# Optimization experiments

Measured on AMD Instinct MI355X. Metric: run time of the kernel, lower is better.

Reference implementation:

```python
import jax, jax.numpy as jnp
import numpy as np

B = 262144      # batch
DIN = 100       # input covariate dim (cfg_density[0][0])
H = 64          # hidden dim
G = 10          # num_grid -> density output dim G+1
NH = 5          # number of dosage-bucket heads in Multi_head


def setup_inputs() -> dict:
    key = jax.random.key(0)
    ks = jax.random.split(key, 16)
    s = 0.05
    return {
        "dosage": jax.random.uniform(ks[0], (B,), dtype=jnp.float32),
        "x": jax.random.normal(ks[1], (B, DIN), dtype=jnp.float32),
        # density feature MLP (two Linear+ReLU layers)
        "dW0": jax.random.normal(ks[2], (DIN, H), dtype=jnp.float32) * s,
        "db0": jax.random.normal(ks[3], (H,), dtype=jnp.float32) * s,
        "dW1": jax.random.normal(ks[4], (H, H), dtype=jnp.float32) * s,
        "db1": jax.random.normal(ks[5], (H,), dtype=jnp.float32) * s,
        # Density_Block: Linear(H -> G+1) then softmax + grid interpolation
        "dbW": jax.random.normal(ks[6], (H, G + 1), dtype=jnp.float32) * s,
        "dbB": jax.random.normal(ks[7], (G + 1,), dtype=jnp.float32) * s,
        # Multi_head: 5 structurally identical heads, params stacked on axis 0
        # layer0: Treat_Linear(64 -> 64, relu, istreat=1)
        "W0": jax.random.normal(ks[8], (NH, H, H), dtype=jnp.float32) * s,
        "tw0": jax.random.normal(ks[9], (NH, H), dtype=jnp.float32) * s,
        "b0": jax.random.normal(ks[10], (NH, H), dtype=jnp.float32) * s,
        # layer1 (last): Treat_Linear(64 -> 1, no act, istreat=1)
        "W1": jax.random.normal(ks[11], (NH, H, 1), dtype=jnp.float32) * s,
        "tw1": jax.random.normal(ks[12], (NH, 1), dtype=jnp.float32) * s,
        "b1": jax.random.normal(ks[13], (NH, 1), dtype=jnp.float32) * s,
    }


def reference(dosage, x, dW0, db0, dW1, db1, dbW, dbB, W0, tw0, b0, W1, tw1, b1):
    # hidden feature MLP
    hidden = jax.nn.relu(x @ dW0 + db0)
    hidden = jax.nn.relu(hidden @ dW1 + db1)            # [B, H]

    # ---- Density_Block: softmax over grid, dual gather + linear interpolation
    p = jax.nn.softmax(hidden @ dbW + dbB, axis=1)      # [B, G+1]
    tB = dosage * G
    U = jnp.ceil(tB)
    inter = 1.0 - (U - tB)                              # fractional position in cell
    Ui = U.astype(jnp.int32)
    Li = Ui - 1
    Li = Li + (Li < 0).astype(jnp.int32)                # clamp L=-1 -> 0
    pL = jnp.take_along_axis(p, Li[:, None], axis=1)[:, 0]
    pU = jnp.take_along_axis(p, Ui[:, None], axis=1)[:, 0]
    g = pL + (pU - pL) * inter                          # [B]

    # ---- Multi_head: 5 heads on dosage buckets [0,.2),[.2,.4),...,[.8,1.)
    t = dosage
    # layer0: out = feat @ W + t * tw + b, relu; compute all heads, select later
    h0 = jax.nn.relu(
        jnp.einsum('bi,hio->bho', hidden, W0)
        + t[:, None, None] * tw0[None]
        + b0[None]
    )                                                   # [B, NH, H]
    # last layer: no activation
    out1 = (jnp.einsum('bho,hoj->bhj', h0, W1)
            + t[:, None, None] * tw1[None]
            + b1[None])                                 # [B, NH, 1]
    bucket = jnp.clip(jnp.floor(t * NH).astype(jnp.int32), 0, NH - 1)
    Q = jnp.take_along_axis(out1, bucket[:, None, None], axis=1)[:, 0, :]  # [B, 1]
    return g, Q
```

## Files before the change

### kernel.cpp

```cpp
#include <hip/hip_runtime.h>

typedef __attribute__((ext_vector_type(8))) short  short8;
typedef __attribute__((ext_vector_type(4))) float  floatx4;
typedef __attribute__((ext_vector_type(4))) int    intx4;

constexpr int DIN = 100;
constexpr int H   = 64;
constexpr int G   = 10;
constexpr int NH  = 5;
constexpr int MWG = 128;
constexpr int HP  = 72;
constexpr int PBP = 20;

constexpr int NF_DW0 = 16, NF_DW1 = 8, NF_DBW = 2;
constexpr int NF_LIN = NF_DW0 + NF_DW1 + NF_DBW;
constexpr int NF_TOT = NF_LIN + 40;

__device__ __forceinline__ unsigned short f2bf_rne(float f) {
    union { float f; unsigned u; } v{f};
    unsigned r = v.u + 0x7FFF + ((v.u >> 16) & 1);
    return (unsigned short)(r >> 16);
}

__device__ __forceinline__ short8 pack8(const float* f) {
    intx4 p;
    #pragma unroll
    for (int j = 0; j < 4; ++j) {
        unsigned a = __float_as_uint(f[2 * j])     + 0x8000u;
        unsigned b = __float_as_uint(f[2 * j + 1]) + 0x8000u;
        p[j] = (int)((b & 0xFFFF0000u) | (a >> 16));
    }
    union { intx4 i; short8 s; } u; u.i = p;
    return u.s;
}

__device__ __forceinline__ unsigned pack2bf(float a, float b) {
    unsigned ua = __float_as_uint(a) + 0x8000u;
    unsigned ub = __float_as_uint(b) + 0x8000u;
    return (ua >> 16) | (ub & 0xFFFF0000u);
}

__device__ __forceinline__ short8 ldfrag(const unsigned short* __restrict__ ws,
                                         int f, int lane) {
    return *(const short8*)(ws + (size_t)(f * 64 + lane) * 8);
}

__device__ __forceinline__ void bar_lgkm() {
    asm volatile("s_waitcnt lgkmcnt(0)" ::: "memory");
    __builtin_amdgcn_s_barrier();
    asm volatile("" ::: "memory");
}

__global__ __launch_bounds__(64) void pack_kernel(
    const float* __restrict__ dW0, const float* __restrict__ dW1,
    const float* __restrict__ dbW, const float* __restrict__ W0,
    unsigned short* __restrict__ ws)
{
    const int f = blockIdx.x;
    const int lane = threadIdx.x;
    const int q = lane >> 4, cl = lane & 15;
    float v[8];
    if (f < NF_DW0) {
        int c = f >> 2, g = f & 3;
        #pragma unroll
        for (int j = 0; j < 8; ++j) {
            int k = c * 32 + q * 8 + j, n = g * 16 + cl;
            v[j] = (k < DIN) ? dW0[k * H + n] : 0.0f;
        }
    } else if (f < NF_DW0 + NF_DW1) {
        int r = f - NF_DW0; int c = r >> 2, g = r & 3;
        #pragma unroll
        for (int j = 0; j < 8; ++j) {
            int k = c * 32 + q * 8 + j, n = g * 16 + cl;
            v[j] = dW1[k * H + n];
        }
    } else if (f < NF_LIN) {
        int c = f - (NF_DW0 + NF_DW1);
        #pragma unroll
        for (int j = 0; j < 8; ++j) {
            int k = c * 32 + q * 8 + j, n = cl;
            v[j] = (n <= G) ? dbW[k * (G + 1) + n] : 0.0f;
        }
    } else {
        int r = f - NF_LIN; int h = r >> 3; r &= 7; int c = r >> 2, g = r & 3;
        #pragma unroll
        for (int j = 0; j < 8; ++j) {
            int k = c * 32 + q * 8 + j, n = g * 16 + cl;
            v[j] = W0[(h * H + k) * H + n];
        }
    }
    short8 s;
    #pragma unroll
    for (int j = 0; j < 8; ++j) s[j] = (short)f2bf_rne(v[j]);
    *(short8*)(ws + (size_t)(f * 64 + lane) * 8) = s;
}

__global__ __launch_bounds__(256, 3) void drnet_mfma(
    const float* __restrict__ dosage, const float* __restrict__ x,
    const float* __restrict__ db0, const float* __restrict__ db1,
    const float* __restrict__ dbB,
    const float* __restrict__ tw0, const float* __restrict__ b0,
    const float* __restrict__ W1, const float* __restrict__ tw1,
    const float* __restrict__ b1,
    const unsigned short* __restrict__ wsfrag,
    float* __restrict__ outg, float* __restrict__ outq)
{
    __shared__ unsigned short hbuf[MWG * HP];
    __shared__ float          pbuf[4][16][PBP];
    __shared__ int            perm[MWG];
    __shared__ float          tbuf[MWG];
    __shared__ unsigned char  bkbuf[MWG];
    __shared__ float          qbuf[MWG];
    __shared__ int            hist[NH];
    __shared__ int            offs[NH];

    const int tid  = threadIdx.x;
    const int wave = tid >> 6, lane = tid & 63;
    const int q = lane >> 4, cl = lane & 15;
    const int rowbase = blockIdx.x * MWG + wave * 32;
    unsigned short* hb = hbuf + wave * 32 * HP;

    floatx4 tvs[2];
    #pragma unroll
    for (int mt = 0; mt < 2; ++mt)
        tvs[mt] = *(const floatx4*)(dosage + rowbase + mt * 16 + 4 * q);
    floatx4 xv[2][7];
    #pragma unroll
    for (int mt = 0; mt < 2; ++mt) {
        const float* xr = x + (size_t)(rowbase + mt * 16 + cl) * DIN;
        #pragma unroll
        for (int cch = 0; cch < 3; ++cch) {
            xv[mt][2 * cch]     = *(const floatx4*)(xr + cch * 32 + q * 8);
            xv[mt][2 * cch + 1] = *(const floatx4*)(xr + cch * 32 + q * 8 + 4);
        }
        xv[mt][6] = (q == 0) ? *(const floatx4*)(xr + 96) : (floatx4)0.0f;
    }

    if (tid < NH) hist[tid] = 0;
    bar_lgkm();
    {
        float t8[2][4];
        int   bk8[2][4];
        #pragma unroll
        for (int mt = 0; mt < 2; ++mt)
            #pragma unroll
            for (int r = 0; r < 4; ++r) {
                float t = tvs[mt][r];
                t8[mt][r] = t;
                int bk = (int)floorf(t * (float)NH);
                bk8[mt][r] = min(max(bk, 0), NH - 1);
            }
        if (cl == 0) {
            #pragma unroll
            for (int mt = 0; mt < 2; ++mt)
                #pragma unroll
                for (int r = 0; r < 4; ++r)
                    atomicAdd(&hist[bk8[mt][r]], 1);
        }
        bar_lgkm();
        if (tid == 0) {
            int a = 0;
            #pragma unroll
            for (int h = 0; h < NH; ++h) { offs[h] = a; a += hist[h]; }
        }
        bar_lgkm();
        if (cl == 0) {
            #pragma unroll
            for (int mt = 0; mt < 2; ++mt)
                #pragma unroll
                for (int r = 0; r < 4; ++r) {
                    const int bk  = bk8[mt][r];
                    const int pos = atomicAdd(&offs[bk], 1);
                    perm[pos]  = wave * 32 + mt * 16 + 4 * q + r;
                    tbuf[pos]  = t8[mt][r];
                    bkbuf[pos] = (unsigned char)bk;
                }
        }
    }

    {
        short8 a1[2][4];
        #pragma unroll
        for (int mt = 0; mt < 2; ++mt)
            #pragma unroll
            for (int cch = 0; cch < 4; ++cch) {
                float f[8];
                if (cch < 3) {
                    #pragma unroll
                    for (int j = 0; j < 4; ++j) {
                        f[j]     = xv[mt][2 * cch][j];
                        f[4 + j] = xv[mt][2 * cch + 1][j];
                    }
                } else {
                    #pragma unroll
                    for (int j = 0; j < 4; ++j) {
                        f[j]     = xv[mt][6][j];
                        f[4 + j] = 0.0f;
                    }
                }
                a1[mt][cch] = pack8(f);
            }
        floatx4 acc[2][4];
        #pragma unroll
        for (int mt = 0; mt < 2; ++mt)
            #pragma unroll
            for (int g = 0; g < 4; ++g) acc[mt][g] = (floatx4)0.0f;
        #pragma unroll
        for (int cch = 0; cch < 4; ++cch)
            #pragma unroll
            for (int g = 0; g < 4; ++g) {
                short8 bf = ldfrag(wsfrag, cch * 4 + g, lane);
                acc[0][g] = __builtin_amdgcn_mfma_f32_16x16x32_bf16(bf, a1[0][cch], acc[0][g], 0, 0, 0);
                acc[1][g] = __builtin_amdgcn_mfma_f32_16x16x32_bf16(bf, a1[1][cch], acc[1][g], 0, 0, 0);
            }
        #pragma unroll
        for (int mt = 0; mt < 2; ++mt)
            #pragma unroll
            for (int g = 0; g < 4; ++g) {
                floatx4 bias = *(const floatx4*)(db0 + g * 16 + 4 * q);
                float v0 = fmaxf(acc[mt][g][0] + bias[0], 0.0f);
                float v1 = fmaxf(acc[mt][g][1] + bias[1], 0.0f);
                float v2 = fmaxf(acc[mt][g][2] + bias[2], 0.0f);
                float v3 = fmaxf(acc[mt][g][3] + bias[3], 0.0f);
                *(uint2*)(hb + (size_t)(mt * 16 + cl) * HP + g * 16 + 4 * q) =
                    make_uint2(pack2bf(v0, v1), pack2bf(v2, v3));
            }
    }

    {
        short8 a2[2][2];
        #pragma unroll
        for (int mt = 0; mt < 2; ++mt)
            #pragma unroll
            for (int cch = 0; cch < 2; ++cch)
                a2[mt][cch] = *(const short8*)(hb + (mt * 16 + cl) * HP + cch * 32 + q * 8);
        floatx4 acc[2][4];
        #pragma unroll
        for (int mt = 0; mt < 2; ++mt)
            #pragma unroll
            for (int g = 0; g < 4; ++g) acc[mt][g] = (floatx4)0.0f;
        #pragma unroll
        for (int cch = 0; cch < 2; ++cch)
            #pragma unroll
            for (int g = 0; g < 4; ++g) {
                short8 bf = ldfrag(wsfrag, NF_DW0 + cch * 4 + g, lane);
                acc[0][g] = __builtin_amdgcn_mfma_f32_16x16x32_bf16(bf, a2[0][cch], acc[0][g], 0, 0, 0);
                acc[1][g] = __builtin_amdgcn_mfma_f32_16x16x32_bf16(bf, a2[1][cch], acc[1][g], 0, 0, 0);
            }
        #pragma unroll
        for (int mt = 0; mt < 2; ++mt)
            #pragma unroll
            for (int g = 0; g < 4; ++g) {
                floatx4 bias = *(const floatx4*)(db1 + g * 16 + 4 * q);
                float v0 = fmaxf(acc[mt][g][0] + bias[0], 0.0f);
                float v1 = fmaxf(acc[mt][g][1] + bias[1], 0.0f);
                float v2 = fmaxf(acc[mt][g][2] + bias[2], 0.0f);
                float v3 = fmaxf(acc[mt][g][3] + bias[3], 0.0f);
                *(uint2*)(hb + (size_t)(mt * 16 + cl) * HP + g * 16 + 4 * q) =
                    make_uint2(pack2bf(v0, v1), pack2bf(v2, v3));
            }
    }

    {
        float tden[2];
        #pragma unroll
        for (int mt = 0; mt < 2; ++mt)
            tden[mt] = dosage[rowbase + mt * 16 + cl];
        short8 af[2][2];
        #pragma unroll
        for (int mt = 0; mt < 2; ++mt)
            #pragma unroll
            for (int cch = 0; cch < 2; ++cch)
                af[mt][cch] = *(const short8*)(hb + (mt * 16 + cl) * HP + cch * 32 + q * 8);
        floatx4 accd[2];
        accd[0] = (floatx4)0.0f; accd[1] = (floatx4)0.0f;
        #pragma unroll
        for (int cch = 0; cch < 2; ++cch) {
            short8 bf = ldfrag(wsfrag, NF_DW0 + NF_DW1 + cch, lane);
            #pragma unroll
            for (int mt = 0; mt < 2; ++mt)
                accd[mt] = __builtin_amdgcn_mfma_f32_16x16x32_bf16(bf, af[mt][cch], accd[mt], 0, 0, 0);
        }
        #pragma unroll
        for (int mt = 0; mt < 2; ++mt) {
            floatx4 ev;
            float sp = 0.0f;
            #pragma unroll
            for (int r = 0; r < 4; ++r) {
                const int gd = 4 * q + r;
                float e = (gd <= G) ? __expf(accd[mt][r] + dbB[gd]) : 0.0f;
                ev[r] = e;
                sp += e;
            }
            float s = sp;
            s += __shfl_xor(s, 16); s += __shfl_xor(s, 32);
            *(floatx4*)(&pbuf[wave][cl][4 * q]) = ev;
            const float t  = tden[mt];
            const float tB = t * (float)G;
            const float U  = ceilf(tB);
            const float inter = 1.0f - (U - tB);
            int Ui = (int)U; int Li = Ui - 1; if (Li < 0) Li = 0;
            const float pL = pbuf[wave][cl][Li];
            const float pU = pbuf[wave][cl][Ui];
            if (q == 0)
                outg[rowbase + mt * 16 + cl] = (pL + (pU - pL) * inter) / s;
        }
    }

    __syncthreads();
    {
        short8 ag[2][2];
        int    prow[2], bkme[2], blo[2], bhi[2];
        float  tme[2];
        #pragma unroll
        for (int mt = 0; mt < 2; ++mt) {
            const int base = (wave * 2 + mt) * 16;
            prow[mt] = perm[base + cl];
            ag[mt][0] = *(const short8*)(hbuf + prow[mt] * HP + q * 8);
            ag[mt][1] = *(const short8*)(hbuf + prow[mt] * HP + 32 + q * 8);
            tme[mt]  = tbuf[base + cl];
            bkme[mt] = bkbuf[base + cl];
            blo[mt]  = bkbuf[base];
            bhi[mt]  = bkbuf[base + 15];
        }
        #pragma unroll
        for (int mt = 0; mt < 2; ++mt) {
            float qp = 0.0f;
            #pragma unroll 1
            for (int h = blo[mt]; h <= bhi[mt]; ++h) {
                floatx4 acch[4];
                #pragma unroll
                for (int g = 0; g < 4; ++g) acch[g] = (floatx4)0.0f;
                #pragma unroll
                for (int cch = 0; cch < 2; ++cch)
                    #pragma unroll
                    for (int g = 0; g < 4; ++g) {
                        short8 bf = ldfrag(wsfrag, NF_LIN + h * 8 + cch * 4 + g, lane);
                        acch[g] = __builtin_amdgcn_mfma_f32_16x16x32_bf16(bf, ag[mt][cch], acch[g], 0, 0, 0);
                    }
                if (bkme[mt] == h) {
                    #pragma unroll
                    for (int g = 0; g < 4; ++g) {
                        const int off = h * H + g * 16 + 4 * q;
                        floatx4 tw0v = *(const floatx4*)(tw0 + off);
                        floatx4 b0v  = *(const floatx4*)(b0  + off);
                        floatx4 w1v  = *(const floatx4*)(W1  + off);
                        #pragma unroll
                        for (int r = 0; r < 4; ++r)
                            qp += fmaxf(acch[g][r] + tme[mt] * tw0v[r] + b0v[r], 0.0f) * w1v[r];
                    }
                }
            }
            qp += __shfl_xor(qp, 16); qp += __shfl_xor(qp, 32);
            if (q == 0)
                qbuf[prow[mt]] = qp + tme[mt] * tw1[bkme[mt]] + b1[bkme[mt]];
        }
    }

    __syncthreads();
    if (tid < MWG / 4) {
        floatx4 v = *(const floatx4*)(qbuf + tid * 4);
        *(floatx4*)(outq + blockIdx.x * MWG + tid * 4) = v;
    }
}

extern "C" void kernel_launch(void* const* d_in, const int* in_sizes, int n_in,
                              void* d_out, int out_size, void* d_ws, size_t ws_size,
                              hipStream_t stream) {
    const float* dosage = (const float*)d_in[0];
    const float* x      = (const float*)d_in[1];
    const float* dW0    = (const float*)d_in[2];
    const float* db0    = (const float*)d_in[3];
    const float* dW1    = (const float*)d_in[4];
    const float* db1    = (const float*)d_in[5];
    const float* dbW    = (const float*)d_in[6];
    const float* dbB    = (const float*)d_in[7];
    const float* W0     = (const float*)d_in[8];
    const float* tw0    = (const float*)d_in[9];
    const float* b0     = (const float*)d_in[10];
    const float* W1     = (const float*)d_in[11];
    const float* tw1    = (const float*)d_in[12];
    const float* b1     = (const float*)d_in[13];

    const int Btot = in_sizes[0];
    float* outg = (float*)d_out;
    float* outq = outg + Btot;
    unsigned short* ws = (unsigned short*)d_ws;

    pack_kernel<<<NF_TOT, 64, 0, stream>>>(dW0, dW1, dbW, W0, ws);
    drnet_mfma<<<Btot / MWG, 256, 0, stream>>>(dosage, x, db0, db1, dbB,
                                               tw0, b0, W1, tw1, b1,
                                               ws, outg, outq);
}
```

Measured before the change: 198.7 us.

## Process four row tiles per block with prefetch of next tile's inputs

After: 264.2 us. 33.0% more time.

```diff
diff --git a/kernel.cpp b/kernel.cpp
--- a/kernel.cpp
+++ b/kernel.cpp
@@ -9,6 +9,7 @@
 constexpr int G   = 10;
 constexpr int NH  = 5;
 constexpr int MWG = 128;
+constexpr int TPB = 4;
 constexpr int HP  = 72;
 constexpr int PBP = 20;
 
@@ -117,250 +118,277 @@
     const int tid  = threadIdx.x;
     const int wave = tid >> 6, lane = tid & 63;
     const int q = lane >> 4, cl = lane & 15;
-    const int rowbase = blockIdx.x * MWG + wave * 32;
     unsigned short* hb = hbuf + wave * 32 * HP;
 
+    const int tilebase = blockIdx.x * TPB;
+
     floatx4 tvs[2];
-    #pragma unroll
-    for (int mt = 0; mt < 2; ++mt)
-        tvs[mt] = *(const floatx4*)(dosage + rowbase + mt * 16 + 4 * q);
     floatx4 xv[2][7];
-    #pragma unroll
-    for (int mt = 0; mt < 2; ++mt) {
-        const float* xr = x + (size_t)(rowbase + mt * 16 + cl) * DIN;
-        #pragma unroll
-        for (int cch = 0; cch < 3; ++cch) {
-            xv[mt][2 * cch]     = *(const floatx4*)(xr + cch * 32 + q * 8);
-            xv[mt][2 * cch + 1] = *(const floatx4*)(xr + cch * 32 + q * 8 + 4);
-        }
-        xv[mt][6] = (q == 0) ? *(const floatx4*)(xr + 96) : (floatx4)0.0f;
+    {
+        const int rowbase = tilebase * MWG + wave * 32;
+        #pragma unroll
+        for (int mt = 0; mt < 2; ++mt)
+            tvs[mt] = *(const floatx4*)(dosage + rowbase + mt * 16 + 4 * q);
+        #pragma unroll
+        for (int mt = 0; mt < 2; ++mt) {
+            const float* xr = x + (size_t)(rowbase + mt * 16 + cl) * DIN;
+            #pragma unroll
+            for (int cch = 0; cch < 3; ++cch) {
+                xv[mt][2 * cch]     = *(const floatx4*)(xr + cch * 32 + q * 8);
+                xv[mt][2 * cch + 1] = *(const floatx4*)(xr + cch * 32 + q * 8 + 4);
+            }
+            xv[mt][6] = (q == 0) ? *(const floatx4*)(xr + 96) : (floatx4)0.0f;
+        }
     }
 
-    if (tid < NH) hist[tid] = 0;
-    bar_lgkm();
-    {
-        float t8[2][4];
-        int   bk8[2][4];
-        #pragma unroll
-        for (int mt = 0; mt < 2; ++mt)
-            #pragma unroll
-            for (int r = 0; r < 4; ++r) {
-                float t = tvs[mt][r];
-                t8[mt][r] = t;
-                int bk = (int)floorf(t * (float)NH);
-                bk8[mt][r] = min(max(bk, 0), NH - 1);
-            }
-        if (cl == 0) {
-            #pragma unroll
-            for (int mt = 0; mt < 2; ++mt)
-                #pragma unroll
-                for (int r = 0; r < 4; ++r)
-                    atomicAdd(&hist[bk8[mt][r]], 1);
-        }
+    #pragma unroll 1
+    for (int t = 0; t < TPB; ++t) {
+        const int rowbase = (tilebase + t) * MWG + wave * 32;
+
+        if (tid < NH) hist[tid] = 0;
         bar_lgkm();
-        if (tid == 0) {
-            int a = 0;
-            #pragma unroll
-            for (int h = 0; h < NH; ++h) { offs[h] = a; a += hist[h]; }
-        }
+        {
+            float t8[2][4];
+            int   bk8[2][4];
+            #pragma unroll
+            for (int mt = 0; mt < 2; ++mt)
+                #pragma unroll
+                for (int r = 0; r < 4; ++r) {
+                    float tt = tvs[mt][r];
+                    t8[mt][r] = tt;
+                    int bk = (int)floorf(tt * (float)NH);
+                    bk8[mt][r] = min(max(bk, 0), NH - 1);
+                }
+            if (cl == 0) {
+                #pragma unroll
+                for (int mt = 0; mt < 2; ++mt)
+                    #pragma unroll
+                    for (int r = 0; r < 4; ++r)
+                        atomicAdd(&hist[bk8[mt][r]], 1);
+            }
+            bar_lgkm();
+            if (tid == 0) {
+                int a = 0;
+                #pragma unroll
+                for (int h = 0; h < NH; ++h) { offs[h] = a; a += hist[h]; }
+            }
+            bar_lgkm();
+            if (cl == 0) {
+                #pragma unroll
+                for (int mt = 0; mt < 2; ++mt)
+                    #pragma unroll
+                    for (int r = 0; r < 4; ++r) {
+                        const int bk  = bk8[mt][r];
+                        const int pos = atomicAdd(&offs[bk], 1);
+                        perm[pos]  = wave * 32 + mt * 16 + 4 * q + r;
+                        tbuf[pos]  = t8[mt][r];
+                        bkbuf[pos] = (unsigned char)bk;
+                    }
+            }
+        }
+
+        {
+            short8 a1[2][4];
+            #pragma unroll
+            for (int mt = 0; mt < 2; ++mt)
+                #pragma unroll
+                for (int cch = 0; cch < 4; ++cch) {
+                    float f[8];
+                    if (cch < 3) {
+                        #pragma unroll
+                        for (int j = 0; j < 4; ++j) {
+                            f[j]     = xv[mt][2 * cch][j];
+                            f[4 + j] = xv[mt][2 * cch + 1][j];
+                        }
+                    } else {
+                        #pragma unroll
+                        for (int j = 0; j < 4; ++j) {
+                            f[j]     = xv[mt][6][j];
+                            f[4 + j] = 0.0f;
+                        }
+                    }
+                    a1[mt][cch] = pack8(f);
+                }
+            floatx4 acc[2][4];
+            #pragma unroll
+            for (int mt = 0; mt < 2; ++mt)
+                #pragma unroll
+                for (int g = 0; g < 4; ++g) acc[mt][g] = (floatx4)0.0f;
+            #pragma unroll
+            for (int cch = 0; cch < 4; ++cch)
+                #pragma unroll
+                for (int g = 0; g < 4; ++g) {
+                    short8 bf = ldfrag(wsfrag, cch * 4 + g, lane);
+                    acc[0][g] = __builtin_amdgcn_mfma_f32_16x16x32_bf16(bf, a1[0][cch], acc[0][g], 0, 0, 0);
+                    acc[1][g] = __builtin_amdgcn_mfma_f32_16x16x32_bf16(bf, a1[1][cch], acc[1][g], 0, 0, 0);
+                }
+            #pragma unroll
+            for (int mt = 0; mt < 2; ++mt)
+                #pragma unroll
+                for (int g = 0; g < 4; ++g) {
+                    floatx4 bias = *(const floatx4*)(db0 + g * 16 + 4 * q);
+                    float v0 = fmaxf(acc[mt][g][0] + bias[0], 0.0f);
+                    float v1 = fmaxf(acc[mt][g][1] + bias[1], 0.0f);
+                    float v2 = fmaxf(acc[mt][g][2] + bias[2], 0.0f);
+                    float v3 = fmaxf(acc[mt][g][3] + bias[3], 0.0f);
+                    *(uint2*)(hb + (size_t)(mt * 16 + cl) * HP + g * 16 + 4 * q) =
+                        make_uint2(pack2bf(v0, v1), pack2bf(v2, v3));
+                }
+        }
+
+        {
+            short8 a2[2][2];
+            #pragma unroll
+            for (int mt = 0; mt < 2; ++mt)
+                #pragma unroll
+                for (int cch = 0; cch < 2; ++cch)
+                    a2[mt][cch] = *(const short8*)(hb + (mt * 16 + cl) * HP + cch * 32 + q * 8);
+            floatx4 acc[2][4];
+            #pragma unroll
+            for (int mt = 0; mt < 2; ++mt)
+                #pragma unroll
+                for (int g = 0; g < 4; ++g) acc[mt][g] = (floatx4)0.0f;
+            #pragma unroll
+            for (int cch = 0; cch < 2; ++cch)
+                #pragma unroll
+                for (int g = 0; g < 4; ++g) {
+                    short8 bf = ldfrag(wsfrag, NF_DW0 + cch * 4 + g, lane);
+                    acc[0][g] = __builtin_amdgcn_mfma_f32_16x16x32_bf16(bf, a2[0][cch], acc[0][g], 0, 0, 0);
+                    acc[1][g] = __builtin_amdgcn_mfma_f32_16x16x32_bf16(bf, a2[1][cch], acc[1][g], 0, 0, 0);
+                }
+            #pragma unroll
+            for (int mt = 0; mt < 2; ++mt)
+                #pragma unroll
+                for (int g = 0; g < 4; ++g) {
+                    floatx4 bias = *(const floatx4*)(db1 + g * 16 + 4 * q);
+                    float v0 = fmaxf(acc[mt][g][0] + bias[0], 0.0f);
+                    float v1 = fmaxf(acc[mt][g][1] + bias[1], 0.0f);
+                    float v2 = fmaxf(acc[mt][g][2] + bias[2], 0.0f);
+                    float v3 = fmaxf(acc[mt][g][3] + bias[3], 0.0f);
+                    *(uint2*)(hb + (size_t)(mt * 16 + cl) * HP + g * 16 + 4 * q) =
+                        make_uint2(pack2bf(v0, v1), pack2bf(v2, v3));
+                }
+        }
+
+        {
+            float tden[2];
+            #pragma unroll
+            for (int mt = 0; mt < 2; ++mt)
+                tden[mt] = dosage[rowbase + mt * 16 + cl];
+            short8 af[2][2];
+            #pragma unroll
+            for (int mt = 0; mt < 2; ++mt)
+                #pragma unroll
+                for (int cch = 0; cch < 2; ++cch)
+                    af[mt][cch] = *(const short8*)(hb + (mt * 16 + cl) * HP + cch * 32 + q * 8);
+            floatx4 accd[2];
+            accd[0] = (floatx4)0.0f; accd[1] = (floatx4)0.0f;
+            #pragma unroll
+            for (int cch = 0; cch < 2; ++cch) {
+                short8 bf = ldfrag(wsfrag, NF_DW0 + NF_DW1 + cch, lane);
+                #pragma unroll
+                for (int mt = 0; mt < 2; ++mt)
+                    accd[mt] = __builtin_amdgcn_mfma_f32_16x16x32_bf16(bf, af[mt][cch], accd[mt], 0, 0, 0);
+            }
+            #pragma unroll
+            for (int mt = 0; mt < 2; ++mt) {
+                floatx4 ev;
+                float sp = 0.0f;
+                #pragma unroll
+                for (int r = 0; r < 4; ++r) {
+                    const int gd = 4 * q + r;
+                    float e = (gd <= G) ? __expf(accd[mt][r] + dbB[gd]) : 0.0f;
+                    ev[r] = e;
+                    sp += e;
+                }
+                float s = sp;
+                s += __shfl_xor(s, 16); s += __shfl_xor(s, 32);
+                *(floatx4*)(&pbuf[wave][cl][4 * q]) = ev;
+                const float tt = tden[mt];
+                const float tB = tt * (float)G;
+                const float U  = ceilf(tB);
+                const float inter = 1.0f - (U - tB);
+                int Ui = (int)U; int Li = Ui - 1; if (Li < 0) Li = 0;
+                const float pL = pbuf[wave][cl][Li];
+                const float pU = pbuf[wave][cl][Ui];
+                if (q == 0)
+                    outg[rowbase + mt * 16 + cl] = (pL + (pU - pL) * inter) / s;
+            }
+        }
+
         bar_lgkm();
-        if (cl == 0) {
-            #pragma unroll
-            for (int mt = 0; mt < 2; ++mt)
-                #pragma unroll
-                for (int r = 0; r < 4; ++r) {
-                    const int bk  = bk8[mt][r];
-                    const int pos = atomicAdd(&offs[bk], 1);
-                    perm[pos]  = wave * 32 + mt * 16 + 4 * q + r;
-                    tbuf[pos]  = t8[mt][r];
-                    bkbuf[pos] = (unsigned char)bk;
-                }
-        }
-    }
-
-    {
-        short8 a1[2][4];
-        #pragma unroll
-        for (int mt = 0; mt < 2; ++mt)
-            #pragma unroll
-            for (int cch = 0; cch < 4; ++cch) {
-                float f[8];
-                if (cch < 3) {
+
+        if (t + 1 < TPB) {
+            const int rbn = rowbase + MWG;
+            #pragma unroll
+            for (int mt = 0; mt < 2; ++mt)
+                tvs[mt] = *(const floatx4*)(dosage + rbn + mt * 16 + 4 * q);
+            #pragma unroll
+            for (int mt = 0; mt < 2; ++mt) {
+                const float* xr = x + (size_t)(rbn + mt * 16 + cl) * DIN;
+                #pragma unroll
+                for (int cch = 0; cch < 3; ++cch) {
+                    xv[mt][2 * cch]     = *(const floatx4*)(xr + cch * 32 + q * 8);
+                    xv[mt][2 * cch + 1] = *(const floatx4*)(xr + cch * 32 + q * 8 + 4);
+                }
+                xv[mt][6] = (q == 0) ? *(const floatx4*)(xr + 96) : (floatx4)0.0f;
+            }
+        }
+
+        {
+            short8 ag[2][2];
+            int    prow[2], bkme[2], blo[2], bhi[2];
+            float  tme[2];
+            #pragma unroll
+            for (int mt = 0; mt < 2; ++mt) {
+                const int base = (wave * 2 + mt) * 16;
+                prow[mt] = perm[base + cl];
+                ag[mt][0] = *(const short8*)(hbuf + prow[mt] * HP + q * 8);
+                ag[mt][1] = *(const short8*)(hbuf + prow[mt] * HP + 32 + q * 8);
+                tme[mt]  = tbuf[base + cl];
+                bkme[mt] = bkbuf[base + cl];
+                blo[mt]  = bkbuf[base];
+                bhi[mt]  = bkbuf[base + 15];
+            }
+            #pragma unroll
+            for (int mt = 0; mt < 2; ++mt) {
+                float qp = 0.0f;
+                #pragma unroll 1
+                for (int h = blo[mt]; h <= bhi[mt]; ++h) {
+                    floatx4 acch[4];
                     #pragma unroll
-                    for (int j = 0; j < 4; ++j) {
-                        f[j]     = xv[mt][2 * cch][j];
-                        f[4 + j] = xv[mt][2 * cch + 1][j];
+                    for (int g = 0; g < 4; ++g) acch[g] = (floatx4)0.0f;
+                    #pragma unroll
+                    for (int cch = 0; cch < 2; ++cch)
+                        #pragma unroll
+                        for (int g = 0; g < 4; ++g) {
+                            short8 bf = ldfrag(wsfrag, NF_LIN + h * 8 + cch * 4 + g, lane);
+                            acch[g] = __builtin_amdgcn_mfma_f32_16x16x32_bf16(bf, ag[mt][cch], acch[g], 0, 0, 0);
+                        }
+                    if (bkme[mt] == h) {
+                        #pragma unroll
+                        for (int g = 0; g < 4; ++g) {
+                            const int off = h * H + g * 16 + 4 * q;
+                            floatx4 tw0v = *(const floatx4*)(tw0 + off);
+                            floatx4 b0v  = *(const floatx4*)(b0  + off);
+                            floatx4 w1v  = *(const floatx4*)(W1  + off);
+                            #pragma unroll
+                            for (int r = 0; r < 4; ++r)
+                                qp += fmaxf(acch[g][r] + tme[mt] * tw0v[r] + b0v[r], 0.0f) * w1v[r];
+                        }
                     }
-                } else {
-                    #pragma unroll
-                    for (int j = 0; j < 4; ++j) {
-                        f[j]     = xv[mt][6][j];
-                        f[4 + j] = 0.0f;
-                    }
-                }
-                a1[mt][cch] = pack8(f);
-            }
-        floatx4 acc[2][4];
-        #pragma unroll
-        for (int mt = 0; mt < 2; ++mt)
-            #pragma unroll
-            for (int g = 0; g < 4; ++g) acc[mt][g] = (floatx4)0.0f;
-        #pragma unroll
-        for (int cch = 0; cch < 4; ++cch)
-            #pragma unroll
-            for (int g = 0; g < 4; ++g) {
-                short8 bf = ldfrag(wsfrag, cch * 4 + g, lane);
-                acc[0][g] = __builtin_amdgcn_mfma_f32_16x16x32_bf16(bf, a1[0][cch], acc[0][g], 0, 0, 0);
-                acc[1][g] = __builtin_amdgcn_mfma_f32_16x16x32_bf16(bf, a1[1][cch], acc[1][g], 0, 0, 0);
-            }
-        #pragma unroll
-        for (int mt = 0; mt < 2; ++mt)
-            #pragma unroll
-            for (int g = 0; g < 4; ++g) {
-                floatx4 bias = *(const floatx4*)(db0 + g * 16 + 4 * q);
-                float v0 = fmaxf(acc[mt][g][0] + bias[0], 0.0f);
-                float v1 = fmaxf(acc[mt][g][1] + bias[1], 0.0f);
-                float v2 = fmaxf(acc[mt][g][2] + bias[2], 0.0f);
-                float v3 = fmaxf(acc[mt][g][3] + bias[3], 0.0f);
-                *(uint2*)(hb + (size_t)(mt * 16 + cl) * HP + g * 16 + 4 * q) =
-                    make_uint2(pack2bf(v0, v1), pack2bf(v2, v3));
-            }
-    }
-
-    {
-        short8 a2[2][2];
-        #pragma unroll
-        for (int mt = 0; mt < 2; ++mt)
-            #pragma unroll
-            for (int cch = 0; cch < 2; ++cch)
-                a2[mt][cch] = *(const short8*)(hb + (mt * 16 + cl) * HP + cch * 32 + q * 8);
-        floatx4 acc[2][4];
-        #pragma unroll
-        for (int mt = 0; mt < 2; ++mt)
-            #pragma unroll
-            for (int g = 0; g < 4; ++g) acc[mt][g] = (floatx4)0.0f;
-        #pragma unroll
-        for (int cch = 0; cch < 2; ++cch)
-            #pragma unroll
-            for (int g = 0; g < 4; ++g) {
-                short8 bf = ldfrag(wsfrag, NF_DW0 + cch * 4 + g, lane);
-                acc[0][g] = __builtin_amdgcn_mfma_f32_16x16x32_bf16(bf, a2[0][cch], acc[0][g], 0, 0, 0);
-                acc[1][g] = __builtin_amdgcn_mfma_f32_16x16x32_bf16(bf, a2[1][cch], acc[1][g], 0, 0, 0);
-            }
-        #pragma unroll
-        for (int mt = 0; mt < 2; ++mt)
-            #pragma unroll
-            for (int g = 0; g < 4; ++g) {
-                floatx4 bias = *(const floatx4*)(db1 + g * 16 + 4 * q);
-                float v0 = fmaxf(acc[mt][g][0] + bias[0], 0.0f);
-                float v1 = fmaxf(acc[mt][g][1] + bias[1], 0.0f);
-                float v2 = fmaxf(acc[mt][g][2] + bias[2], 0.0f);
-                float v3 = fmaxf(acc[mt][g][3] + bias[3], 0.0f);
-                *(uint2*)(hb + (size_t)(mt * 16 + cl) * HP + g * 16 + 4 * q) =
-                    make_uint2(pack2bf(v0, v1), pack2bf(v2, v3));
-            }
-    }
-
-    {
-        float tden[2];
-        #pragma unroll
-        for (int mt = 0; mt < 2; ++mt)
-            tden[mt] = dosage[rowbase + mt * 16 + cl];
-        short8 af[2][2];
-        #pragma unroll
-        for (int mt = 0; mt < 2; ++mt)
-            #pragma unroll
-            for (int cch = 0; cch < 2; ++cch)
-                af[mt][cch] = *(const short8*)(hb + (mt * 16 + cl) * HP + cch * 32 + q * 8);
-        floatx4 accd[2];
-        accd[0] = (floatx4)0.0f; accd[1] = (floatx4)0.0f;
-        #pragma unroll
-        for (int cch = 0; cch < 2; ++cch) {
-            short8 bf = ldfrag(wsfrag, NF_DW0 + NF_DW1 + cch, lane);
-            #pragma unroll
-            for (int mt = 0; mt < 2; ++mt)
-                accd[mt] = __builtin_amdgcn_mfma_f32_16x16x32_bf16(bf, af[mt][cch], accd[mt], 0, 0, 0);
-        }
-        #pragma unroll
-        for (int mt = 0; mt < 2; ++mt) {
-            floatx4 ev;
-            float sp = 0.0f;
-            #pragma unroll
-            for (int r = 0; r < 4; ++r) {
-                const int gd = 4 * q + r;
-                float e = (gd <= G) ? __expf(accd[mt][r] + dbB[gd]) : 0.0f;
-                ev[r] = e;
-                sp += e;
-            }
-            float s = sp;
-            s += __shfl_xor(s, 16); s += __shfl_xor(s, 32);
-            *(floatx4*)(&pbuf[wave][cl][4 * q]) = ev;
-            const float t  = tden[mt];
-            const float tB = t * (float)G;
-            const float U  = ceilf(tB);
-            const float inter = 1.0f - (U - tB);
-            int Ui = (int)U; int Li = Ui - 1; if (Li < 0) Li = 0;
-            const float pL = pbuf[wave][cl][Li];
-            const float pU = pbuf[wave][cl][Ui];
-            if (q == 0)
-                outg[rowbase + mt * 16 + cl] = (pL + (pU - pL) * inter) / s;
-        }
-    }
-
-    __syncthreads();
-    {
-        short8 ag[2][2];
-        int    prow[2], bkme[2], blo[2], bhi[2];
-        float  tme[2];
-        #pragma unroll
-        for (int mt = 0; mt < 2; ++mt) {
-            const int base = (wave * 2 + mt) * 16;
-            prow[mt] = perm[base + cl];
-            ag[mt][0] = *(const short8*)(hbuf + prow[mt] * HP + q * 8);
-            ag[mt][1] = *(const short8*)(hbuf + prow[mt] * HP + 32 + q * 8);
-            tme[mt]  = tbuf[base + cl];
-            bkme[mt] = bkbuf[base + cl];
-            blo[mt]  = bkbuf[base];
-            bhi[mt]  = bkbuf[base + 15];
-        }
-        #pragma unroll
-        for (int mt = 0; mt < 2; ++mt) {
-            float qp = 0.0f;
-            #pragma unroll 1
-            for (int h = blo[mt]; h <= bhi[mt]; ++h) {
-                floatx4 acch[4];
-                #pragma unroll
-                for (int g = 0; g < 4; ++g) acch[g] = (floatx4)0.0f;
-                #pragma unroll
-                for (int cch = 0; cch < 2; ++cch)
-                    #pragma unroll
-                    for (int g = 0; g < 4; ++g) {
-                        short8 bf = ldfrag(wsfrag, NF_LIN + h * 8 + cch * 4 + g, lane);
-                        acch[g] = __builtin_amdgcn_mfma_f32_16x16x32_bf16(bf, ag[mt][cch], acch[g], 0, 0, 0);
-                    }
-                if (bkme[mt] == h) {
-                    #pragma unroll
-                    for (int g = 0; g < 4; ++g) {
-                        const int off = h * H + g * 16 + 4 * q;
-                        floatx4 tw0v = *(const floatx4*)(tw0 + off);
-                        floatx4 b0v  = *(const floatx4*)(b0  + off);
-                        floatx4 w1v  = *(const floatx4*)(W1  + off);
-                        #pragma unroll
-                        for (int r = 0; r < 4; ++r)
-                            qp += fmaxf(acch[g][r] + tme[mt] * tw0v[r] + b0v[r], 0.0f) * w1v[r];
-                    }
-                }
-            }
-            qp += __shfl_xor(qp, 16); qp += __shfl_xor(qp, 32);
-            if (q == 0)
-                qbuf[prow[mt]] = qp + tme[mt] * tw1[bkme[mt]] + b1[bkme[mt]];
-        }
-    }
-
-    __syncthreads();
-    if (tid < MWG / 4) {
-        floatx4 v = *(const floatx4*)(qbuf + tid * 4);
-        *(floatx4*)(outq + blockIdx.x * MWG + tid * 4) = v;
+                }
+                qp += __shfl_xor(qp, 16); qp += __shfl_xor(qp, 32);
+                if (q == 0)
+                    qbuf[prow[mt]] = qp + tme[mt] * tw1[bkme[mt]] + b1[bkme[mt]];
+            }
+        }
+
+        bar_lgkm();
+        if (tid < MWG / 4) {
+            floatx4 v = *(const floatx4*)(qbuf + tid * 4);
+            *(floatx4*)(outq + (tilebase + t) * MWG + tid * 4) = v;
+        }
     }
 }
 
@@ -388,7 +416,7 @@
     unsigned short* ws = (unsigned short*)d_ws;
 
     pack_kernel<<<NF_TOT, 64, 0, stream>>>(dW0, dW1, dbW, W0, ws);
-    drnet_mfma<<<Btot / MWG, 256, 0, stream>>>(dosage, x, db0, db1, dbB,
-                                               tw0, b0, W1, tw1, b1,
-                                               ws, outg, outq);
-}
+    drnet_mfma<<<Btot / (MWG * TPB), 256, 0, stream>>>(dosage, x, db0, db1, dbB,
+                                                       tw0, b0, W1, tw1, b1,
+                                                       ws, outg, outq);
+}
```

## Replace block-wide atomic bucket sort with per-wave ballot sort, drop barriers

Applied to the files above, without the earlier changes.

Result: slower. 228.0 us (+14.8%).

```diff
diff --git a/kernel.cpp b/kernel.cpp
--- a/kernel.cpp
+++ b/kernel.cpp
@@ -43,12 +43,6 @@
 __device__ __forceinline__ short8 ldfrag(const unsigned short* __restrict__ ws,
                                          int f, int lane) {
     return *(const short8*)(ws + (size_t)(f * 64 + lane) * 8);
-}
-
-__device__ __forceinline__ void bar_lgkm() {
-    asm volatile("s_waitcnt lgkmcnt(0)" ::: "memory");
-    __builtin_amdgcn_s_barrier();
-    asm volatile("" ::: "memory");
 }
 
 __global__ __launch_bounds__(64) void pack_kernel(
@@ -95,7 +89,7 @@
     *(short8*)(ws + (size_t)(f * 64 + lane) * 8) = s;
 }
 
-__global__ __launch_bounds__(256, 3) void drnet_mfma(
+__global__ __launch_bounds__(256, 6) void drnet_mfma(
     const float* __restrict__ dosage, const float* __restrict__ x,
     const float* __restrict__ db0, const float* __restrict__ db1,
     const float* __restrict__ dbB,
@@ -105,25 +99,19 @@
     const unsigned short* __restrict__ wsfrag,
     float* __restrict__ outg, float* __restrict__ outq)
 {
-    __shared__ unsigned short hbuf[MWG * HP];
+    __shared__ unsigned short hbuf[4][32 * HP];
     __shared__ float          pbuf[4][16][PBP];
-    __shared__ int            perm[MWG];
-    __shared__ float          tbuf[MWG];
-    __shared__ unsigned char  bkbuf[MWG];
-    __shared__ float          qbuf[MWG];
-    __shared__ int            hist[NH];
-    __shared__ int            offs[NH];
+    __shared__ int            perm[4][32];
+    __shared__ float          tbufs[4][32];
+    __shared__ int            bks[4][32];
+    __shared__ float          qbufs[4][32];
 
     const int tid  = threadIdx.x;
     const int wave = tid >> 6, lane = tid & 63;
     const int q = lane >> 4, cl = lane & 15;
     const int rowbase = blockIdx.x * MWG + wave * 32;
-    unsigned short* hb = hbuf + wave * 32 * HP;
-
-    floatx4 tvs[2];
-    #pragma unroll
-    for (int mt = 0; mt < 2; ++mt)
-        tvs[mt] = *(const floatx4*)(dosage + rowbase + mt * 16 + 4 * q);
+    unsigned short* hb = hbuf[wave];
+
     floatx4 xv[2][7];
     #pragma unroll
     for (int mt = 0; mt < 2; ++mt) {
@@ -136,45 +124,28 @@
         xv[mt][6] = (q == 0) ? *(const floatx4*)(xr + 96) : (floatx4)0.0f;
     }
 
-    if (tid < NH) hist[tid] = 0;
-    bar_lgkm();
-    {
-        float t8[2][4];
-        int   bk8[2][4];
-        #pragma unroll
-        for (int mt = 0; mt < 2; ++mt)
-            #pragma unroll
-            for (int r = 0; r < 4; ++r) {
-                float t = tvs[mt][r];
-                t8[mt][r] = t;
-                int bk = (int)floorf(t * (float)NH);
-                bk8[mt][r] = min(max(bk, 0), NH - 1);
-            }
-        if (cl == 0) {
-            #pragma unroll
-            for (int mt = 0; mt < 2; ++mt)
-                #pragma unroll
-                for (int r = 0; r < 4; ++r)
-                    atomicAdd(&hist[bk8[mt][r]], 1);
-        }
-        bar_lgkm();
-        if (tid == 0) {
-            int a = 0;
-            #pragma unroll
-            for (int h = 0; h < NH; ++h) { offs[h] = a; a += hist[h]; }
-        }
-        bar_lgkm();
-        if (cl == 0) {
-            #pragma unroll
-            for (int mt = 0; mt < 2; ++mt)
-                #pragma unroll
-                for (int r = 0; r < 4; ++r) {
-                    const int bk  = bk8[mt][r];
-                    const int pos = atomicAdd(&offs[bk], 1);
-                    perm[pos]  = wave * 32 + mt * 16 + 4 * q + r;
-                    tbuf[pos]  = t8[mt][r];
-                    bkbuf[pos] = (unsigned char)bk;
-                }
+    {
+        const int row = lane & 31;
+        const float tl = dosage[rowbase + row];
+        int bk = (int)floorf(tl * (float)NH);
+        bk = min(max(bk, 0), NH - 1);
+        const unsigned m0 = (unsigned)__ballot(bk == 0);
+        const unsigned m1 = (unsigned)__ballot(bk == 1);
+        const unsigned m2 = (unsigned)__ballot(bk == 2);
+        const unsigned m3 = (unsigned)__ballot(bk == 3);
+        const unsigned m4 = (unsigned)__ballot(bk == 4);
+        int base = 0;
+        base += (bk > 0) ? __popc(m0) : 0;
+        base += (bk > 1) ? __popc(m1) : 0;
+        base += (bk > 2) ? __popc(m2) : 0;
+        base += (bk > 3) ? __popc(m3) : 0;
+        const unsigned mymask = (bk == 0) ? m0 : (bk == 1) ? m1 :
+                                (bk == 2) ? m2 : (bk == 3) ? m3 : m4;
+        const int pos = base + __popc(mymask & ((1u << row) - 1u));
+        if (lane < 32) {
+            perm[wave][pos]  = row;
+            tbufs[wave][pos] = tl;
+            bks[wave][pos]   = bk;
         }
     }
 
@@ -295,8 +266,8 @@
             float s = sp;
             s += __shfl_xor(s, 16); s += __shfl_xor(s, 32);
             *(floatx4*)(&pbuf[wave][cl][4 * q]) = ev;
-            const float t  = tden[mt];
-            const float tB = t * (float)G;
+            const float tt = tden[mt];
+            const float tB = tt * (float)G;
             const float U  = ceilf(tB);
             const float inter = 1.0f - (U - tB);
             int Ui = (int)U; int Li = Ui - 1; if (Li < 0) Li = 0;
@@ -307,21 +278,20 @@
         }
     }
 
-    __syncthreads();
     {
         short8 ag[2][2];
         int    prow[2], bkme[2], blo[2], bhi[2];
         float  tme[2];
         #pragma unroll
         for (int mt = 0; mt < 2; ++mt) {
-            const int base = (wave * 2 + mt) * 16;
-            prow[mt] = perm[base + cl];
-            ag[mt][0] = *(const short8*)(hbuf + prow[mt] * HP + q * 8);
-            ag[mt][1] = *(const short8*)(hbuf + prow[mt] * HP + 32 + q * 8);
-            tme[mt]  = tbuf[base + cl];
-            bkme[mt] = bkbuf[base + cl];
-            blo[mt]  = bkbuf[base];
-            bhi[mt]  = bkbuf[base + 15];
+            const int base = mt * 16;
+            prow[mt] = perm[wave][base + cl];
+            ag[mt][0] = *(const short8*)(hb + prow[mt] * HP + q * 8);
+            ag[mt][1] = *(const short8*)(hb + prow[mt] * HP + 32 + q * 8);
+            tme[mt]  = tbufs[wave][base + cl];
+            bkme[mt] = bks[wave][base + cl];
+            blo[mt]  = bks[wave][base];
+            bhi[mt]  = bks[wave][base + 15];
         }
         #pragma unroll
         for (int mt = 0; mt < 2; ++mt) {
@@ -353,14 +323,13 @@
             }
             qp += __shfl_xor(qp, 16); qp += __shfl_xor(qp, 32);
             if (q == 0)
-                qbuf[prow[mt]] = qp + tme[mt] * tw1[bkme[mt]] + b1[bkme[mt]];
-        }
-    }
-
-    __syncthreads();
-    if (tid < MWG / 4) {
-        floatx4 v = *(const floatx4*)(qbuf + tid * 4);
-        *(floatx4*)(outq + blockIdx.x * MWG + tid * 4) = v;
+                qbufs[wave][prow[mt]] = qp + tme[mt] * tw1[bkme[mt]] + b1[bkme[mt]];
+        }
+    }
+
+    if (lane < 8) {
+        floatx4 v = *(const floatx4*)(&qbufs[wave][lane * 4]);
+        *(floatx4*)(outq + rowbase + lane * 4) = v;
     }
 }
 
```
